# Performance work log

Hardware: AMD Instinct MI355X
Metric: run time of the kernel (lower is better)

Reference implementation:

```python
import jax, jax.numpy as jnp
import numpy as np

NUM_CLASSES = 80
MASK_SIZE = 3
ATTRIBS = 5 + NUM_CLASSES
NET_W = 608.0
NET_H = 608.0
# Faithful to the original indexing bug: anchor_w = masked_anchors[a], anchor_h = masked_anchors[a+1]
MASKED_ANCHORS = np.array([10.0, 13.0, 16.0, 30.0, 33.0, 23.0], dtype=np.float32)
ANCHOR_W = jnp.asarray(MASKED_ANCHORS[0:MASK_SIZE])      # [10, 13, 16]
ANCHOR_H = jnp.asarray(MASKED_ANCHORS[1:MASK_SIZE + 1])  # [13, 16, 30]


def setup_inputs() -> dict:
    key = jax.random.key(0)
    x = jax.random.normal(key, (16, MASK_SIZE * ATTRIBS, 76, 76), dtype=jnp.float32)
    return {"x": x}


def reference(x):
    B, C, H, W = x.shape
    # (B, A, attribs, H, W) -> (B, A, H, W, attribs)
    pred = x.reshape(B, MASK_SIZE, ATTRIBS, H, W).transpose(0, 1, 3, 4, 2)
    tx = jax.nn.sigmoid(pred[..., 0])
    ty = jax.nn.sigmoid(pred[..., 1])
    tw = pred[..., 2]
    th = pred[..., 3]
    conf = jax.nn.sigmoid(pred[..., 4])
    pred_cls = jax.nn.sigmoid(pred[..., 5:])

    gi = jnp.arange(W, dtype=x.dtype)[None, None, None, :]  # column index i
    gj = jnp.arange(H, dtype=x.dtype)[None, None, :, None]  # row index j
    bx = (gi + tx) / W
    by = (gj + ty) / H
    bw = jnp.exp(tw) * ANCHOR_W[None, :, None, None] / NET_W
    bh = jnp.exp(th) * ANCHOR_H[None, :, None, None] / NET_H

    boxes = jnp.stack([bx, by, bw, bh], axis=-1)  # (B, A, H, W, 4)
    # (B, A, H, W, 4+1+num_classes)
    return jnp.concatenate([boxes, conf[..., None], pred_cls], axis=-1)
```

## Files before the change

kernel.cpp:

```cpp
#include <hip/hip_runtime.h>
#include <stdint.h>

#define NB      16
#define NA      3
#define HH_     76
#define WW_     76
#define S_TOT   (HH_ * WW_)
#define ATTR    85
#define TILE_S  76
#define TILES   (S_TOT / TILE_S)
#define CHUNKS4 (TILE_S / 4)
#define UNITS   (ATTR * CHUNKS4)
#define NTHREADS 256
#define NBATCH  7
#define LOG2E   1.44269504088896340f

typedef __attribute__((ext_vector_type(4))) float float4v;

__device__ __forceinline__ float fast_sigmoid(float x) {
    float e = __builtin_amdgcn_exp2f(x * (-LOG2E));
    return __builtin_amdgcn_rcpf(1.0f + e);
}

__global__ __launch_bounds__(NTHREADS)
void yolo_layer_kernel(const float* __restrict__ in,
                       float* __restrict__ out) {
    __shared__ __attribute__((aligned(16))) float lds[TILE_S * ATTR];

    const int tid  = threadIdx.x;
    const int tile = blockIdx.x;
    const int BA   = blockIdx.y;
    const int a    = BA % NA;
    const int s0   = tile * TILE_S;

    const float aw = (a == 0) ? 10.0f : (a == 1) ? 13.0f : 16.0f;
    const float ah = (a == 0) ? 13.0f : (a == 1) ? 16.0f : 30.0f;
    const float cw = aw * (1.0f / 608.0f);
    const float ch = ah * (1.0f / 608.0f);

    const float* inb = in + (size_t)BA * (ATTR * S_TOT) + s0;

    float4v v[NBATCH];
    #pragma unroll
    for (int i = 0; i < NBATCH; ++i) {
        int u  = tid + i * NTHREADS;
        int uc = (u < UNITS) ? u : 0;
        int k  = uc / CHUNKS4;
        int c  = uc - k * CHUNKS4;
        v[i] = *(const float4v*)(inb + (size_t)k * S_TOT + c * 4);
    }

    #pragma unroll
    for (int i = 0; i < NBATCH; ++i) {
        int u = tid + i * NTHREADS;
        if (u >= UNITS) break;
        int k  = u / CHUNKS4;
        int c  = u - k * CHUNKS4;
        int sl = c * 4;

        float r[4];
        if (k >= 4) {
            #pragma unroll
            for (int j = 0; j < 4; ++j) r[j] = fast_sigmoid(v[i][j]);
        } else {
            #pragma unroll
            for (int j = 0; j < 4; ++j) {
                float x  = v[i][j];
                int   sp = s0 + sl + j;
                int   hy = sp / WW_;
                int   wx = sp - hy * WW_;
                if      (k == 0) r[j] = ((float)wx + fast_sigmoid(x)) * (1.0f / 76.0f);
                else if (k == 1) r[j] = ((float)hy + fast_sigmoid(x)) * (1.0f / 76.0f);
                else if (k == 2) r[j] = __builtin_amdgcn_exp2f(x * LOG2E) * cw;
                else             r[j] = __builtin_amdgcn_exp2f(x * LOG2E) * ch;
            }
        }

        float* lp = &lds[sl * ATTR + k];
        #pragma unroll
        for (int j = 0; j < 4; ++j) lp[j * ATTR] = r[j];
    }

    __syncthreads();

    float4v* outv = (float4v*)(out + ((size_t)BA * S_TOT + s0) * ATTR);
    const float4v* ldsv = (const float4v*)lds;

    float4v w[NBATCH];
    #pragma unroll
    for (int i = 0; i < NBATCH; ++i) {
        int u  = tid + i * NTHREADS;
        int uc = (u < UNITS) ? u : 0;
        w[i] = ldsv[uc];
    }
    #pragma unroll
    for (int i = 0; i < NBATCH; ++i) {
        int u = tid + i * NTHREADS;
        if (u >= UNITS) break;
        __builtin_nontemporal_store(w[i], &outv[u]);
    }
}

extern "C" void kernel_launch(void* const* d_in, const int* in_sizes, int n_in,
                              void* d_out, int out_size, void* d_ws, size_t ws_size,
                              hipStream_t stream) {
    const float* in = (const float*)d_in[0];
    float* out = (float*)d_out;

    dim3 grid(TILES, NB * NA);
    dim3 block(NTHREADS);
    yolo_layer_kernel<<<grid, block, 0, stream>>>(in, out);
}
```

Measured before the change: 170.6 us.

## Load scalar attribute quads per position and double tile size with 512 threads

Each thread now owns one spatial position and four consecutive attributes, loaded as four scalar coalesced reads, in place of a float4 along the spatial axis. This makes the LDS writes contiguous per thread instead of strided by 85, which is meant to cut LDS bank conflicts. The box branch becomes uniform per quad group. The tile grows to 152 positions with 512 threads, halving the grid and doubling LDS per block, which may lower occupancy. Global loads become 4-byte instead of 16-byte vectors.

```diff
diff --git a/kernel.cpp b/kernel.cpp
--- a/kernel.cpp
+++ b/kernel.cpp
@@ -1,19 +1,21 @@
 #include <hip/hip_runtime.h>
 #include <stdint.h>
 
-#define NB      16
-#define NA      3
-#define HH_     76
-#define WW_     76
-#define S_TOT   (HH_ * WW_)
-#define ATTR    85
-#define TILE_S  76
-#define TILES   (S_TOT / TILE_S)
-#define CHUNKS4 (TILE_S / 4)
-#define UNITS   (ATTR * CHUNKS4)
-#define NTHREADS 256
-#define NBATCH  7
-#define LOG2E   1.44269504088896340f
+#define NB       16
+#define NA       3
+#define HH_      76
+#define WW_      76
+#define S_TOT    (HH_ * WW_)
+#define ATTR     85
+#define TILE_S   152
+#define TILES    (S_TOT / TILE_S)
+#define NTHREADS 512
+#define QUADS    22
+#define UNITS1   (QUADS * TILE_S)
+#define UNITS2   (TILE_S * ATTR / 4)
+#define NB1      7
+#define NB2      7
+#define LOG2E    1.44269504088896340f
 
 typedef __attribute__((ext_vector_type(4))) float float4v;
 
@@ -40,45 +42,48 @@
 
     const float* inb = in + (size_t)BA * (ATTR * S_TOT) + s0;
 
-    float4v v[NBATCH];
+    float v[NB1][4];
     #pragma unroll
-    for (int i = 0; i < NBATCH; ++i) {
+    for (int i = 0; i < NB1; ++i) {
         int u  = tid + i * NTHREADS;
-        int uc = (u < UNITS) ? u : 0;
-        int k  = uc / CHUNKS4;
-        int c  = uc - k * CHUNKS4;
-        v[i] = *(const float4v*)(inb + (size_t)k * S_TOT + c * 4);
+        int uc = (u < UNITS1) ? u : 0;
+        int g  = uc / TILE_S;
+        int s  = uc - g * TILE_S;
+        const float* p = inb + s;
+        #pragma unroll
+        for (int q = 0; q < 4; ++q) {
+            int k = 4 * g + q;
+            if (k > ATTR - 1) k = ATTR - 1;
+            v[i][q] = p[(size_t)k * S_TOT];
+        }
     }
 
     #pragma unroll
-    for (int i = 0; i < NBATCH; ++i) {
+    for (int i = 0; i < NB1; ++i) {
         int u = tid + i * NTHREADS;
-        if (u >= UNITS) break;
-        int k  = u / CHUNKS4;
-        int c  = u - k * CHUNKS4;
-        int sl = c * 4;
+        if (u >= UNITS1) break;
+        int g = u / TILE_S;
+        int s = u - g * TILE_S;
 
         float r[4];
-        if (k >= 4) {
+        if (g != 0) {
             #pragma unroll
-            for (int j = 0; j < 4; ++j) r[j] = fast_sigmoid(v[i][j]);
+            for (int q = 0; q < 4; ++q) r[q] = fast_sigmoid(v[i][q]);
         } else {
-            #pragma unroll
-            for (int j = 0; j < 4; ++j) {
-                float x  = v[i][j];
-                int   sp = s0 + sl + j;
-                int   hy = sp / WW_;
-                int   wx = sp - hy * WW_;
-                if      (k == 0) r[j] = ((float)wx + fast_sigmoid(x)) * (1.0f / 76.0f);
-                else if (k == 1) r[j] = ((float)hy + fast_sigmoid(x)) * (1.0f / 76.0f);
-                else if (k == 2) r[j] = __builtin_amdgcn_exp2f(x * LOG2E) * cw;
-                else             r[j] = __builtin_amdgcn_exp2f(x * LOG2E) * ch;
-            }
+            int sp = s0 + s;
+            int hy = sp / WW_;
+            int wx = sp - hy * WW_;
+            r[0] = ((float)wx + fast_sigmoid(v[i][0])) * (1.0f / 76.0f);
+            r[1] = ((float)hy + fast_sigmoid(v[i][1])) * (1.0f / 76.0f);
+            r[2] = __builtin_amdgcn_exp2f(v[i][2] * LOG2E) * cw;
+            r[3] = __builtin_amdgcn_exp2f(v[i][3] * LOG2E) * ch;
         }
 
-        float* lp = &lds[sl * ATTR + k];
+        float* lp = &lds[s * ATTR + 4 * g];
         #pragma unroll
-        for (int j = 0; j < 4; ++j) lp[j * ATTR] = r[j];
+        for (int q = 0; q < 4; ++q) {
+            if (4 * g + q < ATTR) lp[q] = r[q];
+        }
     }
 
     __syncthreads();
@@ -86,17 +91,17 @@
     float4v* outv = (float4v*)(out + ((size_t)BA * S_TOT + s0) * ATTR);
     const float4v* ldsv = (const float4v*)lds;
 
-    float4v w[NBATCH];
+    float4v w[NB2];
     #pragma unroll
-    for (int i = 0; i < NBATCH; ++i) {
+    for (int i = 0; i < NB2; ++i) {
         int u  = tid + i * NTHREADS;
-        int uc = (u < UNITS) ? u : 0;
+        int uc = (u < UNITS2) ? u : 0;
         w[i] = ldsv[uc];
     }
     #pragma unroll
-    for (int i = 0; i < NBATCH; ++i) {
+    for (int i = 0; i < NB2; ++i) {
         int u = tid + i * NTHREADS;
-        if (u >= UNITS) break;
+        if (u >= UNITS2) break;
         __builtin_nontemporal_store(w[i], &outv[u]);
     }
 }
```

Result: no change. 168.6 us (-1.1%).
